# Kernel tuning notes

Hardware: AMD Instinct MI355X
Metric: run time of the kernel (lower is better)

Reference implementation:

```python
import jax, jax.numpy as jnp
import numpy as np

N_NODES = 50000
N_EDGES = 800000
F_NODE = 128
F_EDGE = 32
H = 64


def _gat_layer(x, row, col, e_emb, W, le_W, att_src, att_dst, att_edge, bias):
    """PyG GATConv (heads=1, concat=True) with edge_dim, incl. self loops.
    x: [N, Fin]; row/col: [E] int (src, dst); e_emb: [E, H].
    """
    N = x.shape[0]
    loop = jnp.arange(N, dtype=row.dtype)
    row_a = jnp.concatenate([row, loop])
    col_a = jnp.concatenate([col, loop])
    # self-loop edge attr = mean of edge embeddings (PyG fill_value='mean')
    e_mean = jnp.mean(e_emb, axis=0)
    e_all = jnp.concatenate([e_emb, jnp.broadcast_to(e_mean, (N, e_emb.shape[1]))], axis=0)

    h = x @ W.T                      # [N, H]
    a_src = h @ att_src              # [N]
    a_dst = h @ att_dst              # [N]
    a_edge = (e_all @ le_W.T) @ att_edge  # [E+N]

    alpha = jax.nn.leaky_relu(a_src[row_a] + a_dst[col_a] + a_edge, negative_slope=0.2)
    # segment softmax over destination node neighborhoods
    m = jax.ops.segment_max(alpha, col_a, num_segments=N)
    ex = jnp.exp(alpha - m[col_a])
    denom = jax.ops.segment_sum(ex, col_a, num_segments=N)
    w = ex / denom[col_a]            # [E+N]
    out = jax.ops.segment_sum(h[row_a] * w[:, None], col_a, num_segments=N)
    return out + bias


def setup_inputs() -> dict:
    key = jax.random.key(0)
    ks = jax.random.split(key, 20)
    s = 0.1
    inp = {
        "x": jax.random.normal(ks[0], (N_NODES, F_NODE), dtype=jnp.float32),
        "edge_attr": jax.random.normal(ks[1], (N_EDGES, F_EDGE), dtype=jnp.float32),
        "edge_index": jax.random.randint(ks[2], (2, N_EDGES), 0, N_NODES, dtype=jnp.int32),
        # edge encoder (Linear with bias)
        "enc_W": jax.random.normal(ks[3], (H, F_EDGE), dtype=jnp.float32) * s,
        "enc_b": jnp.zeros((H,), dtype=jnp.float32),
        # conv1 params
        "W1": jax.random.normal(ks[4], (H, F_NODE), dtype=jnp.float32) * s,
        "le1_W": jax.random.normal(ks[5], (H, H), dtype=jnp.float32) * s,
        "as1": jax.random.normal(ks[6], (H,), dtype=jnp.float32) * s,
        "ad1": jax.random.normal(ks[7], (H,), dtype=jnp.float32) * s,
        "ae1": jax.random.normal(ks[8], (H,), dtype=jnp.float32) * s,
        "b1": jnp.zeros((H,), dtype=jnp.float32),
        # conv2 params
        "W2": jax.random.normal(ks[9], (H, H), dtype=jnp.float32) * s,
        "le2_W": jax.random.normal(ks[10], (H, H), dtype=jnp.float32) * s,
        "as2": jax.random.normal(ks[11], (H,), dtype=jnp.float32) * s,
        "ad2": jax.random.normal(ks[12], (H,), dtype=jnp.float32) * s,
        "ae2": jax.random.normal(ks[13], (H,), dtype=jnp.float32) * s,
        "b2": jnp.zeros((H,), dtype=jnp.float32),
        # edge scorer MLP: Linear(2H, H) -> ReLU -> Linear(H, 1)
        "s1_W": jax.random.normal(ks[14], (H, 2 * H), dtype=jnp.float32) * s,
        "s1_b": jnp.zeros((H,), dtype=jnp.float32),
        "s2_W": jax.random.normal(ks[15], (1, H), dtype=jnp.float32) * s,
        "s2_b": jnp.zeros((1,), dtype=jnp.float32),
    }
    return inp


def reference(x, edge_attr, edge_index, enc_W, enc_b,
              W1, le1_W, as1, ad1, ae1, b1,
              W2, le2_W, as2, ad2, ae2, b2,
              s1_W, s1_b, s2_W, s2_b):
    row, col = edge_index[0], edge_index[1]
    edge_emb = edge_attr @ enc_W.T + enc_b           # [E, H]
    h = jax.nn.relu(_gat_layer(x, row, col, edge_emb, W1, le1_W, as1, ad1, ae1, b1))
    # dropout p=0.5 is identity in eval mode
    h = _gat_layer(h, row, col, edge_emb, W2, le2_W, as2, ad2, ae2, b2)
    ef = jnp.concatenate([h[row], h[col]], axis=1)   # [E, 2H]
    z = jax.nn.relu(ef @ s1_W.T + s1_b) @ s2_W.T + s2_b  # [E, 1]
    return jax.nn.sigmoid(z).squeeze(-1)             # [E]
```

## Files before the change

### kernel.cpp

```cpp
#include <hip/hip_runtime.h>
#include <cstdint>
#include <cstddef>

#define NN 50000
#define NE 800000
#define FN 128
#define FE 32
#define HD 64
#define SCAN_NB ((NN + 255) / 256)

__device__ __forceinline__ float lrelu(float x) { return x > 0.f ? x : 0.2f * x; }

__global__ void k_small0(const float* __restrict__ le1W, const float* __restrict__ ae1,
                         const float* __restrict__ le2W, const float* __restrict__ ae2,
                         const float* __restrict__ encW, const float* __restrict__ encb,
                         const float* __restrict__ s1W,
                         float* __restrict__ small, float* __restrict__ Scomb) {
  __shared__ float sv1[64], sv2[64];
  int t = threadIdx.x;
  float v1 = 0.f, v2 = 0.f;
  for (int j = 0; j < 64; ++j) {
    v1 += le1W[j * 64 + t] * ae1[j];
    v2 += le2W[j * 64 + t] * ae2[j];
  }
  sv1[t] = v1; sv2[t] = v2;
  small[t] = v1; small[64 + t] = v2;
  float cb1 = encb[t] * v1, cb2 = encb[t] * v2;
  #pragma unroll
  for (int m = 32; m; m >>= 1) { cb1 += __shfl_xor(cb1, m); cb2 += __shfl_xor(cb2, m); }
  __syncthreads();
  if (t < 32) {
    float p1 = 0.f, p2 = 0.f;
    for (int i = 0; i < 64; ++i) {
      p1 += encW[i * 32 + t] * sv1[i];
      p2 += encW[i * 32 + t] * sv2[i];
    }
    small[128 + t] = p1; small[160 + t] = p2;
  }
  if (t == 0) { small[192] = cb1; small[193] = cb2; }
  for (int j = 0; j < 64; ++j) {
    Scomb[j * 64 + t] = s1W[j * 128 + t];
    Scomb[(64 + j) * 64 + t] = s1W[j * 128 + 64 + t];
  }
}

__global__ __launch_bounds__(256) void k_scanA(const int* __restrict__ counts,
                                               int* __restrict__ loc, int* __restrict__ blocksums) {
  int tid = threadIdx.x;
  int i = blockIdx.x * 256 + tid;
  int v = (i < NN) ? counts[i] : 0;
  int lane = tid & 63, wid = tid >> 6;
  int x = v;
  #pragma unroll
  for (int d = 1; d < 64; d <<= 1) {
    int y = __shfl_up(x, d);
    if (lane >= d) x += y;
  }
  __shared__ int ws[4], wpref[4];
  if (lane == 63) ws[wid] = x;
  __syncthreads();
  if (tid == 0) {
    int run = 0;
    #pragma unroll
    for (int w = 0; w < 4; ++w) { wpref[w] = run; run += ws[w]; }
    blocksums[blockIdx.x] = run;
  }
  __syncthreads();
  if (i < NN) loc[i] = x - v + wpref[wid];
}

__global__ __launch_bounds__(256) void k_scanB(int* __restrict__ blocksums, int* __restrict__ offa,
                                               float* __restrict__ small) {
  int tid = threadIdx.x;
  int v = (tid < SCAN_NB) ? blocksums[tid] : 0;
  int lane = tid & 63, wid = tid >> 6;
  int x = v;
  #pragma unroll
  for (int d = 1; d < 64; d <<= 1) {
    int y = __shfl_up(x, d);
    if (lane >= d) x += y;
  }
  __shared__ int ws[4], wpref[4];
  if (lane == 63) ws[wid] = x;
  __syncthreads();
  if (tid == 0) {
    int run = 0;
    #pragma unroll
    for (int w = 0; w < 4; ++w) { wpref[w] = run; run += ws[w]; }
    offa[NN] = run;
    small[194] = small[228] * (1.0f / NE);
    small[195] = small[229] * (1.0f / NE);
  }
  __syncthreads();
  if (tid < SCAN_NB) blocksums[tid] = x - v + wpref[wid];
}

__global__ __launch_bounds__(256) void k_scanC(int* __restrict__ offa, const int* __restrict__ blocksums) {
  int i = blockIdx.x * 256 + threadIdx.x;
  if (i < NN) offa[i] = offa[i] + blocksums[blockIdx.x];
}

__global__ __launch_bounds__(256) void k_edgepre(const float* __restrict__ attr,
                                                 const int* __restrict__ col,
                                                 const float* __restrict__ small,
                                                 float* __restrict__ a_e1, float* __restrict__ a_e2,
                                                 int* __restrict__ rank,
                                                 int* __restrict__ counts,
                                                 float* __restrict__ sums) {
  __shared__ float sattr[256 * 33];
  __shared__ float redbuf[8];
  int tid = threadIdx.x;
  float sp1[32], sp2[32];
  #pragma unroll
  for (int j = 0; j < 8; ++j) {
    float4 v1 = ((const float4*)(small + 128))[j];
    float4 v2 = ((const float4*)(small + 160))[j];
    sp1[j*4+0] = v1.x; sp1[j*4+1] = v1.y; sp1[j*4+2] = v1.z; sp1[j*4+3] = v1.w;
    sp2[j*4+0] = v2.x; sp2[j*4+1] = v2.y; sp2[j*4+2] = v2.z; sp2[j*4+3] = v2.w;
  }
  float c1 = small[192], c2 = small[193];
  const float4* ain = (const float4*)(attr + (size_t)blockIdx.x * 256 * FE);
  #pragma unroll
  for (int it = 0; it < 8; ++it) {
    int idx = it * 256 + tid;
    float4 v = ain[idx];
    int r = idx >> 3, ch = idx & 7;
    float* dst = &sattr[r * 33 + ch * 4];
    dst[0] = v.x; dst[1] = v.y; dst[2] = v.z; dst[3] = v.w;
  }
  __syncthreads();
  const float* myrow = &sattr[tid * 33];
  float d1 = c1, d2 = c2;
  #pragma unroll
  for (int j = 0; j < 32; ++j) {
    float a = myrow[j];
    d1 += a * sp1[j];
    d2 += a * sp2[j];
  }
  int e = blockIdx.x * 256 + tid;
  a_e1[e] = d1;
  a_e2[e] = d2;
  int c = col[e];
  rank[e] = atomicAdd(&counts[c], 1);
  float s1 = d1, s2 = d2;
  #pragma unroll
  for (int m = 32; m; m >>= 1) { s1 += __shfl_xor(s1, m); s2 += __shfl_xor(s2, m); }
  int wid = tid >> 6;
  if ((tid & 63) == 0) { redbuf[wid] = s1; redbuf[4 + wid] = s2; }
  __syncthreads();
  if (tid == 0) atomicAdd(&sums[0], redbuf[0] + redbuf[1] + redbuf[2] + redbuf[3]);
  if (tid == 1) atomicAdd(&sums[1], redbuf[4] + redbuf[5] + redbuf[6] + redbuf[7]);
}

__global__ __launch_bounds__(256) void k_scatter(const int* __restrict__ row, const int* __restrict__ col,
                                                 const float* __restrict__ a_e1, const float* __restrict__ a_e2,
                                                 const int* __restrict__ rank, const int* __restrict__ offa,
                                                 int4* __restrict__ pk) {
  int e = blockIdx.x * 256 + threadIdx.x;
  int c = col[e];
  int p = offa[c] + rank[e];
  int4 q;
  q.x = row[e];
  q.y = __float_as_int(a_e1[e]);
  q.z = __float_as_int(a_e2[e]);
  q.w = 0;
  pk[p] = q;
}

template <int K, int ASD>
__global__ __launch_bounds__(256) void k_gemm(const float* __restrict__ A, const float* __restrict__ B,
                                              float* __restrict__ C, int M, int ldc,
                                              const float* __restrict__ as, const float* __restrict__ ad,
                                              float* __restrict__ asrc, float* __restrict__ adst) {
  __shared__ float At[64][68];
  __shared__ float Bt[64][68];
  int tid = threadIdx.x;
  int m0 = blockIdx.x * 64;
  const float* Bp = B + (size_t)blockIdx.y * 64 * K;
  float acc[4][4] = {};
  for (int kc = 0; kc < K; kc += 64) {
    #pragma unroll
    for (int it = 0; it < 4; ++it) {
      int idx = it * 256 + tid;
      int m = idx & 63, kv = idx >> 6;
      float4 bv = ((const float4*)(Bp + (size_t)m * K + kc))[kv];
      Bt[kv*4+0][m] = bv.x; Bt[kv*4+1][m] = bv.y; Bt[kv*4+2][m] = bv.z; Bt[kv*4+3][m] = bv.w;
      int gm = m0 + m;
      float4 av = make_float4(0.f, 0.f, 0.f, 0.f);
      if (gm < M) av = ((const float4*)(A + (size_t)gm * K + kc))[kv];
      At[kv*4+0][m] = av.x; At[kv*4+1][m] = av.y; At[kv*4+2][m] = av.z; At[kv*4+3][m] = av.w;
    }
    __syncthreads();
    int tn = tid & 15, tm = tid >> 4;
    #pragma unroll 8
    for (int k = 0; k < 64; ++k) {
      float4 a4 = *(const float4*)&At[k][tm * 4];
      float4 b4 = *(const float4*)&Bt[k][tn * 4];
      acc[0][0] += a4.x*b4.x; acc[0][1] += a4.x*b4.y; acc[0][2] += a4.x*b4.z; acc[0][3] += a4.x*b4.w;
      acc[1][0] += a4.y*b4.x; acc[1][1] += a4.y*b4.y; acc[1][2] += a4.y*b4.z; acc[1][3] += a4.y*b4.w;
      acc[2][0] += a4.z*b4.x; acc[2][1] += a4.z*b4.y; acc[2][2] += a4.z*b4.z; acc[2][3] += a4.z*b4.w;
      acc[3][0] += a4.w*b4.x; acc[3][1] += a4.w*b4.y; acc[3][2] += a4.w*b4.z; acc[3][3] += a4.w*b4.w;
    }
    __syncthreads();
  }
  int tn = tid & 15, tm = tid >> 4;
  #pragma unroll
  for (int i = 0; i < 4; ++i) {
    int gm = m0 + tm * 4 + i;
    if (gm < M) {
      float4 o = make_float4(acc[i][0], acc[i][1], acc[i][2], acc[i][3]);
      *(float4*)(C + (size_t)gm * ldc + blockIdx.y * 64 + tn * 4) = o;
    }
  }
  if constexpr (ASD) {
    float4 asv = ((const float4*)as)[tn];
    float4 adv = ((const float4*)ad)[tn];
    #pragma unroll
    for (int i = 0; i < 4; ++i) {
      float s = acc[i][0]*asv.x + acc[i][1]*asv.y + acc[i][2]*asv.z + acc[i][3]*asv.w;
      float d = acc[i][0]*adv.x + acc[i][1]*adv.y + acc[i][2]*adv.z + acc[i][3]*adv.w;
      #pragma unroll
      for (int m = 8; m; m >>= 1) { s += __shfl_xor(s, m, 16); d += __shfl_xor(d, m, 16); }
      int gm = m0 + tm * 4 + i;
      if (tn == 0 && gm < M) { asrc[gm] = s; adst[gm] = d; }
    }
  }
}

__global__ __launch_bounds__(256) void k_agg(const float* __restrict__ h, const int* __restrict__ offa,
                                             const int4* __restrict__ pk, int comp,
                                             const float* __restrict__ asrc, const float* __restrict__ adst,
                                             const float* __restrict__ small, int selfIdx,
                                             const float* __restrict__ bias, float* __restrict__ outp,
                                             int do_relu) {
  int gt = blockIdx.x * 256 + threadIdx.x;
  int n = gt >> 6, lane = gt & 63;
  if (n >= NN) return;
  int beg = offa[n], end = offa[n + 1];
  float a_self = small[selfIdx];
  float adn = adst[n];
  float alpha_self = lrelu(asrc[n] + adn + a_self);
  float mx = alpha_self;
  for (int base = beg; base < end; base += 64) {
    int p = base + lane;
    if (p < end) {
      int4 q = pk[p];
      float ae = __int_as_float(comp ? q.z : q.y);
      float al = lrelu(asrc[q.x] + adn + ae);
      mx = fmaxf(mx, al);
    }
  }
  #pragma unroll
  for (int m = 32; m; m >>= 1) mx = fmaxf(mx, __shfl_xor(mx, m));
  float ex_self = __expf(alpha_self - mx);
  float denom = ex_self;
  float acc = ex_self * h[(size_t)n * 64 + lane];
  for (int base = beg; base < end; base += 64) {
    int p = base + lane;
    int cnt = min(64, end - base);
    float ex = 0.f; int s = 0;
    if (p < end) {
      int4 q = pk[p];
      s = q.x;
      float ae = __int_as_float(comp ? q.z : q.y);
      ex = __expf(lrelu(asrc[s] + adn + ae) - mx);
    }
    float exs = ex;
    #pragma unroll
    for (int m = 32; m; m >>= 1) exs += __shfl_xor(exs, m);
    denom += exs;
    for (int q = 0; q < cnt; ++q) {
      float exq = __shfl(ex, q);
      int sq = __shfl(s, q);
      acc += exq * h[(size_t)sq * 64 + lane];
    }
  }
  float r = acc / denom + bias[lane];
  if (do_relu) r = fmaxf(r, 0.f);
  outp[(size_t)n * 64 + lane] = r;
}

__global__ __launch_bounds__(256) void k_final(const int* __restrict__ row, const int* __restrict__ col,
                                               const float* __restrict__ uv, const float* __restrict__ s1b,
                                               const float* __restrict__ s2w, const float* __restrict__ s2b,
                                               float* __restrict__ outp) {
  int gt = blockIdx.x * 256 + threadIdx.x;
  int e = gt >> 4, i = gt & 15;
  if (e >= NE) return;
  int r = row[e], c = col[e];
  float4 a = ((const float4*)(uv + (size_t)r * 128))[i];
  float4 b = ((const float4*)(uv + (size_t)c * 128 + 64))[i];
  float4 bb = ((const float4*)s1b)[i];
  float4 ww = ((const float4*)s2w)[i];
  float z = fmaxf(a.x + b.x + bb.x, 0.f) * ww.x
          + fmaxf(a.y + b.y + bb.y, 0.f) * ww.y
          + fmaxf(a.z + b.z + bb.z, 0.f) * ww.z
          + fmaxf(a.w + b.w + bb.w, 0.f) * ww.w;
  #pragma unroll
  for (int m = 1; m < 16; m <<= 1) z += __shfl_xor(z, m, 16);
  if (i == 0) outp[e] = 1.f / (1.f + __expf(-(z + s2b[0])));
}

extern "C" void kernel_launch(void* const* d_in, const int* in_sizes, int n_in,
                              void* d_out, int out_size, void* d_ws, size_t ws_size,
                              hipStream_t stream) {
  const float* x    = (const float*)d_in[0];
  const float* attr = (const float*)d_in[1];
  const int*   eidx = (const int*)d_in[2];
  const float* encW = (const float*)d_in[3];
  const float* encb = (const float*)d_in[4];
  const float* W1   = (const float*)d_in[5];
  const float* le1W = (const float*)d_in[6];
  const float* as1  = (const float*)d_in[7];
  const float* ad1  = (const float*)d_in[8];
  const float* ae1w = (const float*)d_in[9];
  const float* b1   = (const float*)d_in[10];
  const float* W2   = (const float*)d_in[11];
  const float* le2W = (const float*)d_in[12];
  const float* as2  = (const float*)d_in[13];
  const float* ad2  = (const float*)d_in[14];
  const float* ae2w = (const float*)d_in[15];
  const float* b2   = (const float*)d_in[16];
  const float* s1W  = (const float*)d_in[17];
  const float* s1b  = (const float*)d_in[18];
  const float* s2w  = (const float*)d_in[19];
  const float* s2b  = (const float*)d_in[20];
  float* outp = (float*)d_out;

  const int* row = eidx;
  const int* col = eidx + NE;

  char* p = (char*)d_ws;
  auto alloc = [&](size_t bytes) { char* r = p; p += (bytes + 255) & ~(size_t)255; return r; };
  float* small = (float*)alloc(1024);
  float* Scomb = (float*)alloc(8192 * 4);
  int*   counts= (int*)alloc((size_t)NN * 4);
  int*   offa  = (int*)alloc((size_t)(NN + 1) * 4);
  int*   bsums = (int*)alloc((size_t)SCAN_NB * 4);
  float* a_e1  = (float*)alloc((size_t)NE * 4);
  float* a_e2  = (float*)alloc((size_t)NE * 4);
  int*   rank  = (int*)alloc((size_t)NE * 4);
  int4*  pk    = (int4*)alloc((size_t)NE * 16);
  float* h1    = (float*)alloc((size_t)NN * 64 * 4);
  float* out1  = (float*)alloc((size_t)NN * 64 * 4);
  float* h2    = (float*)alloc((size_t)NN * 64 * 4);
  float* out2  = (float*)alloc((size_t)NN * 64 * 4);
  float* asrc1 = (float*)alloc((size_t)NN * 4);
  float* adst1 = (float*)alloc((size_t)NN * 4);
  float* asrc2 = (float*)alloc((size_t)NN * 4);
  float* adst2 = (float*)alloc((size_t)NN * 4);
  float* uv = h1;

  hipMemsetAsync(small, 0, 1024, stream);
  hipMemsetAsync(counts, 0, (size_t)NN * 4, stream);

  k_small0<<<1, 64, 0, stream>>>(le1W, ae1w, le2W, ae2w, encW, encb, s1W, small, Scomb);
  k_edgepre<<<NE / 256, 256, 0, stream>>>(attr, col, small, a_e1, a_e2, rank, counts, small + 228);
  k_scanA<<<SCAN_NB, 256, 0, stream>>>(counts, offa, bsums);
  k_scanB<<<1, 256, 0, stream>>>(bsums, offa, small);
  k_scanC<<<SCAN_NB, 256, 0, stream>>>(offa, bsums);
  k_scatter<<<NE / 256, 256, 0, stream>>>(row, col, a_e1, a_e2, rank, offa, pk);

  k_gemm<128, 1><<<dim3((NN + 63) / 64, 1), 256, 0, stream>>>(x, W1, h1, NN, 64, as1, ad1, asrc1, adst1);
  k_agg<<<(NN * 64) / 256, 256, 0, stream>>>(h1, offa, pk, 0, asrc1, adst1,
                                             small, 194, b1, out1, 1);
  k_gemm<64, 1><<<dim3((NN + 63) / 64, 1), 256, 0, stream>>>(out1, W2, h2, NN, 64, as2, ad2, asrc2, adst2);
  k_agg<<<(NN * 64) / 256, 256, 0, stream>>>(h2, offa, pk, 1, asrc2, adst2,
                                             small, 195, b2, out2, 0);
  k_gemm<64, 0><<<dim3((NN + 63) / 64, 2), 256, 0, stream>>>(out2, Scomb, uv, NN, 128, nullptr, nullptr, nullptr, nullptr);
  k_final<<<(NE * 16) / 256, 256, 0, stream>>>(row, col, uv, s1b, s2w, s2b, outp);
}
```

Measured before the change: 368.8 us.

## Replace global atomic rank counting with per-block LDS histograms and prefix reduction

Edge ranking within destination buckets moves out of the edge-preprocessing kernel, where it used global atomics on counts, into a dedicated histogram kernel. Each of 256 blocks builds 16-bit packed shared-memory histograms in two node-range phases, and a node-reduction kernel prefix-sums the per-block histograms to produce counts and per-block offsets. The scatter kernel then combines the block prefix with a local 16-bit rank. This removes contended global atomics and the counts memset, but adds two kernel launches, a 25.6 MB histogram buffer that reuses h1, and a serial 256-step column walk in the reduction kernel.

```diff
diff --git a/kernel.cpp b/kernel.cpp
--- a/kernel.cpp
+++ b/kernel.cpp
@@ -8,6 +8,9 @@
 #define FE 32
 #define HD 64
 #define SCAN_NB ((NN + 255) / 256)
+#define NB_H 256
+#define EPB_H (NE / NB_H)
+#define NWORD 25000
 
 __device__ __forceinline__ float lrelu(float x) { return x > 0.f ? x : 0.2f * x; }
 
@@ -44,6 +47,49 @@
   }
 }
 
+__global__ __launch_bounds__(256) void k_hist(const int* __restrict__ col,
+                                              uint32_t* __restrict__ histg,
+                                              unsigned short* __restrict__ rankw) {
+  __shared__ uint32_t h32[NWORD / 2];
+  int tid = threadIdx.x;
+  int b = blockIdx.x;
+  int e0 = b * EPB_H;
+  #pragma unroll
+  for (int ph = 0; ph < 2; ++ph) {
+    for (int i = tid; i < NWORD / 2; i += 256) h32[i] = 0;
+    __syncthreads();
+    int lo = ph * 25000;
+    for (int i = tid; i < EPB_H; i += 256) {
+      int c = col[e0 + i];
+      unsigned local = (unsigned)(c - lo);
+      if (local < 25000u) {
+        uint32_t sh = (local & 1u) * 16u;
+        uint32_t old = atomicAdd(&h32[local >> 1], 1u << sh);
+        rankw[e0 + i] = (unsigned short)((old >> sh) & 0xffffu);
+      }
+    }
+    __syncthreads();
+    uint32_t* dst = histg + (size_t)b * NWORD + ph * (NWORD / 2);
+    for (int i = tid; i < NWORD / 2; i += 256) dst[i] = h32[i];
+    __syncthreads();
+  }
+}
+
+__global__ __launch_bounds__(256) void k_nodered(uint32_t* __restrict__ histg,
+                                                 int* __restrict__ counts) {
+  int w = blockIdx.x * 256 + threadIdx.x;
+  if (w >= NWORD) return;
+  uint32_t run = 0;
+  for (int b = 0; b < NB_H; ++b) {
+    uint32_t* p = histg + (size_t)b * NWORD + w;
+    uint32_t v = *p;
+    *p = run;
+    run += v;
+  }
+  counts[2 * w] = (int)(run & 0xffffu);
+  counts[2 * w + 1] = (int)(run >> 16);
+}
+
 __global__ __launch_bounds__(256) void k_scanA(const int* __restrict__ counts,
                                                int* __restrict__ loc, int* __restrict__ blocksums) {
   int tid = threadIdx.x;
@@ -101,11 +147,8 @@
 }
 
 __global__ __launch_bounds__(256) void k_edgepre(const float* __restrict__ attr,
-                                                 const int* __restrict__ col,
                                                  const float* __restrict__ small,
                                                  float* __restrict__ a_e1, float* __restrict__ a_e2,
-                                                 int* __restrict__ rank,
-                                                 int* __restrict__ counts,
                                                  float* __restrict__ sums) {
   __shared__ float sattr[256 * 33];
   __shared__ float redbuf[8];
@@ -140,8 +183,6 @@
   int e = blockIdx.x * 256 + tid;
   a_e1[e] = d1;
   a_e2[e] = d2;
-  int c = col[e];
-  rank[e] = atomicAdd(&counts[c], 1);
   float s1 = d1, s2 = d2;
   #pragma unroll
   for (int m = 32; m; m >>= 1) { s1 += __shfl_xor(s1, m); s2 += __shfl_xor(s2, m); }
@@ -154,11 +195,15 @@
 
 __global__ __launch_bounds__(256) void k_scatter(const int* __restrict__ row, const int* __restrict__ col,
                                                  const float* __restrict__ a_e1, const float* __restrict__ a_e2,
-                                                 const int* __restrict__ rank, const int* __restrict__ offa,
+                                                 const unsigned short* __restrict__ rankw,
+                                                 const uint32_t* __restrict__ histg,
+                                                 const int* __restrict__ offa,
                                                  int4* __restrict__ pk) {
   int e = blockIdx.x * 256 + threadIdx.x;
   int c = col[e];
-  int p = offa[c] + rank[e];
+  int b = e / EPB_H;
+  int pre = (int)((const unsigned short*)histg)[(size_t)b * (2 * NWORD) + c];
+  int p = offa[c] + pre + (int)rankw[e];
   int4 q;
   q.x = row[e];
   q.y = __float_as_int(a_e1[e]);
@@ -339,7 +384,7 @@
   int*   bsums = (int*)alloc((size_t)SCAN_NB * 4);
   float* a_e1  = (float*)alloc((size_t)NE * 4);
   float* a_e2  = (float*)alloc((size_t)NE * 4);
-  int*   rank  = (int*)alloc((size_t)NE * 4);
+  unsigned short* rankw = (unsigned short*)alloc((size_t)NE * 2);
   int4*  pk    = (int4*)alloc((size_t)NE * 16);
   float* h1    = (float*)alloc((size_t)NN * 64 * 4);
   float* out1  = (float*)alloc((size_t)NN * 64 * 4);
@@ -350,16 +395,18 @@
   float* asrc2 = (float*)alloc((size_t)NN * 4);
   float* adst2 = (float*)alloc((size_t)NN * 4);
   float* uv = h1;
+  uint32_t* histg = (uint32_t*)h1;
 
   hipMemsetAsync(small, 0, 1024, stream);
-  hipMemsetAsync(counts, 0, (size_t)NN * 4, stream);
 
   k_small0<<<1, 64, 0, stream>>>(le1W, ae1w, le2W, ae2w, encW, encb, s1W, small, Scomb);
-  k_edgepre<<<NE / 256, 256, 0, stream>>>(attr, col, small, a_e1, a_e2, rank, counts, small + 228);
+  k_edgepre<<<NE / 256, 256, 0, stream>>>(attr, small, a_e1, a_e2, small + 228);
+  k_hist<<<NB_H, 256, 0, stream>>>(col, histg, rankw);
+  k_nodered<<<(NWORD + 255) / 256, 256, 0, stream>>>(histg, counts);
   k_scanA<<<SCAN_NB, 256, 0, stream>>>(counts, offa, bsums);
   k_scanB<<<1, 256, 0, stream>>>(bsums, offa, small);
   k_scanC<<<SCAN_NB, 256, 0, stream>>>(offa, bsums);
-  k_scatter<<<NE / 256, 256, 0, stream>>>(row, col, a_e1, a_e2, rank, offa, pk);
+  k_scatter<<<NE / 256, 256, 0, stream>>>(row, col, a_e1, a_e2, rankw, histg, offa, pk);
 
   k_gemm<128, 1><<<dim3((NN + 63) / 64, 1), 256, 0, stream>>>(x, W1, h1, NN, 64, as1, ad1, asrc1, adst1);
   k_agg<<<(NN * 64) / 256, 256, 0, stream>>>(h1, offa, pk, 0, asrc1, adst1,
```

Result: slower. 392.3 us (+6.4%).

## Replace per-node softmax max pass with global upper-bound max from atomics

Applied to the files above, without the earlier changes.

Drops the per-node first pass over incoming edges that computed the exact segment max. Instead, an upper bound on the max is built from global maxima of a_src and a_edge, gathered with ordered-int atomicMax in the GEMM and edge-prep kernels, and passed through leaky ReLU. Softmax is invariant to the shift, so this removes one full gather pass over the edges per layer. It risks underflow in exp when a node's logits sit far below the global bound, and it adds a block sync plus an atomic per GEMM block. The self-loop edge term is not included in the bound.

```diff
diff --git a/kernel.cpp b/kernel.cpp
--- a/kernel.cpp
+++ b/kernel.cpp
@@ -10,6 +10,14 @@
 #define SCAN_NB ((NN + 255) / 256)
 
 __device__ __forceinline__ float lrelu(float x) { return x > 0.f ? x : 0.2f * x; }
+
+__device__ __forceinline__ unsigned omap(float f) {
+  unsigned u = __float_as_uint(f);
+  return (u & 0x80000000u) ? ~u : (u | 0x80000000u);
+}
+__device__ __forceinline__ float odec(unsigned u) {
+  return __uint_as_float((u & 0x80000000u) ? (u ^ 0x80000000u) : ~u);
+}
 
 __global__ void k_small0(const float* __restrict__ le1W, const float* __restrict__ ae1,
                          const float* __restrict__ le2W, const float* __restrict__ ae2,
@@ -106,9 +114,10 @@
                                                  float* __restrict__ a_e1, float* __restrict__ a_e2,
                                                  int* __restrict__ rank,
                                                  int* __restrict__ counts,
-                                                 float* __restrict__ sums) {
+                                                 float* __restrict__ sums,
+                                                 unsigned* __restrict__ maxi) {
   __shared__ float sattr[256 * 33];
-  __shared__ float redbuf[8];
+  __shared__ float redbuf[16];
   int tid = threadIdx.x;
   float sp1[32], sp2[32];
   #pragma unroll
@@ -142,14 +151,19 @@
   a_e2[e] = d2;
   int c = col[e];
   rank[e] = atomicAdd(&counts[c], 1);
-  float s1 = d1, s2 = d2;
-  #pragma unroll
-  for (int m = 32; m; m >>= 1) { s1 += __shfl_xor(s1, m); s2 += __shfl_xor(s2, m); }
+  float s1 = d1, s2 = d2, m1 = d1, m2 = d2;
+  #pragma unroll
+  for (int m = 32; m; m >>= 1) {
+    s1 += __shfl_xor(s1, m); s2 += __shfl_xor(s2, m);
+    m1 = fmaxf(m1, __shfl_xor(m1, m)); m2 = fmaxf(m2, __shfl_xor(m2, m));
+  }
   int wid = tid >> 6;
-  if ((tid & 63) == 0) { redbuf[wid] = s1; redbuf[4 + wid] = s2; }
+  if ((tid & 63) == 0) { redbuf[wid] = s1; redbuf[4 + wid] = s2; redbuf[8 + wid] = m1; redbuf[12 + wid] = m2; }
   __syncthreads();
   if (tid == 0) atomicAdd(&sums[0], redbuf[0] + redbuf[1] + redbuf[2] + redbuf[3]);
   if (tid == 1) atomicAdd(&sums[1], redbuf[4] + redbuf[5] + redbuf[6] + redbuf[7]);
+  if (tid == 2) atomicMax(&maxi[2], omap(fmaxf(fmaxf(redbuf[8], redbuf[9]), fmaxf(redbuf[10], redbuf[11]))));
+  if (tid == 3) atomicMax(&maxi[3], omap(fmaxf(fmaxf(redbuf[12], redbuf[13]), fmaxf(redbuf[14], redbuf[15]))));
 }
 
 __global__ __launch_bounds__(256) void k_scatter(const int* __restrict__ row, const int* __restrict__ col,
@@ -171,7 +185,8 @@
 __global__ __launch_bounds__(256) void k_gemm(const float* __restrict__ A, const float* __restrict__ B,
                                               float* __restrict__ C, int M, int ldc,
                                               const float* __restrict__ as, const float* __restrict__ ad,
-                                              float* __restrict__ asrc, float* __restrict__ adst) {
+                                              float* __restrict__ asrc, float* __restrict__ adst,
+                                              unsigned* __restrict__ maxslot) {
   __shared__ float At[64][68];
   __shared__ float Bt[64][68];
   int tid = threadIdx.x;
@@ -213,8 +228,10 @@
     }
   }
   if constexpr (ASD) {
+    __shared__ float wmax[4];
     float4 asv = ((const float4*)as)[tn];
     float4 adv = ((const float4*)ad)[tn];
+    float smax = -1e30f;
     #pragma unroll
     for (int i = 0; i < 4; ++i) {
       float s = acc[i][0]*asv.x + acc[i][1]*asv.y + acc[i][2]*asv.z + acc[i][3]*asv.w;
@@ -222,8 +239,14 @@
       #pragma unroll
       for (int m = 8; m; m >>= 1) { s += __shfl_xor(s, m, 16); d += __shfl_xor(d, m, 16); }
       int gm = m0 + tm * 4 + i;
-      if (tn == 0 && gm < M) { asrc[gm] = s; adst[gm] = d; }
-    }
+      if (tn == 0 && gm < M) { asrc[gm] = s; adst[gm] = d; smax = fmaxf(smax, s); }
+    }
+    #pragma unroll
+    for (int m = 32; m; m >>= 1) smax = fmaxf(smax, __shfl_xor(smax, m));
+    if ((tid & 63) == 0) wmax[tid >> 6] = smax;
+    __syncthreads();
+    if (tid == 0)
+      atomicMax(maxslot, omap(fmaxf(fmaxf(wmax[0], wmax[1]), fmaxf(wmax[2], wmax[3]))));
   }
 }
 
@@ -231,6 +254,7 @@
                                              const int4* __restrict__ pk, int comp,
                                              const float* __restrict__ asrc, const float* __restrict__ adst,
                                              const float* __restrict__ small, int selfIdx,
+                                             const unsigned* __restrict__ maxi,
                                              const float* __restrict__ bias, float* __restrict__ outp,
                                              int do_relu) {
   int gt = blockIdx.x * 256 + threadIdx.x;
@@ -239,19 +263,8 @@
   int beg = offa[n], end = offa[n + 1];
   float a_self = small[selfIdx];
   float adn = adst[n];
+  float mx = lrelu(odec(maxi[comp]) + adn + odec(maxi[2 + comp]));
   float alpha_self = lrelu(asrc[n] + adn + a_self);
-  float mx = alpha_self;
-  for (int base = beg; base < end; base += 64) {
-    int p = base + lane;
-    if (p < end) {
-      int4 q = pk[p];
-      float ae = __int_as_float(comp ? q.z : q.y);
-      float al = lrelu(asrc[q.x] + adn + ae);
-      mx = fmaxf(mx, al);
-    }
-  }
-  #pragma unroll
-  for (int m = 32; m; m >>= 1) mx = fmaxf(mx, __shfl_xor(mx, m));
   float ex_self = __expf(alpha_self - mx);
   float denom = ex_self;
   float acc = ex_self * h[(size_t)n * 64 + lane];
@@ -333,6 +346,7 @@
   char* p = (char*)d_ws;
   auto alloc = [&](size_t bytes) { char* r = p; p += (bytes + 255) & ~(size_t)255; return r; };
   float* small = (float*)alloc(1024);
+  unsigned* maxi = (unsigned*)alloc(256);
   float* Scomb = (float*)alloc(8192 * 4);
   int*   counts= (int*)alloc((size_t)NN * 4);
   int*   offa  = (int*)alloc((size_t)(NN + 1) * 4);
@@ -352,21 +366,22 @@
   float* uv = h1;
 
   hipMemsetAsync(small, 0, 1024, stream);
+  hipMemsetAsync(maxi, 0, 256, stream);
   hipMemsetAsync(counts, 0, (size_t)NN * 4, stream);
 
   k_small0<<<1, 64, 0, stream>>>(le1W, ae1w, le2W, ae2w, encW, encb, s1W, small, Scomb);
-  k_edgepre<<<NE / 256, 256, 0, stream>>>(attr, col, small, a_e1, a_e2, rank, counts, small + 228);
+  k_edgepre<<<NE / 256, 256, 0, stream>>>(attr, col, small, a_e1, a_e2, rank, counts, small + 228, maxi);
   k_scanA<<<SCAN_NB, 256, 0, stream>>>(counts, offa, bsums);
   k_scanB<<<1, 256, 0, stream>>>(bsums, offa, small);
   k_scanC<<<SCAN_NB, 256, 0, stream>>>(offa, bsums);
   k_scatter<<<NE / 256, 256, 0, stream>>>(row, col, a_e1, a_e2, rank, offa, pk);
 
-  k_gemm<128, 1><<<dim3((NN + 63) / 64, 1), 256, 0, stream>>>(x, W1, h1, NN, 64, as1, ad1, asrc1, adst1);
+  k_gemm<128, 1><<<dim3((NN + 63) / 64, 1), 256, 0, stream>>>(x, W1, h1, NN, 64, as1, ad1, asrc1, adst1, maxi + 0);
   k_agg<<<(NN * 64) / 256, 256, 0, stream>>>(h1, offa, pk, 0, asrc1, adst1,
-                                             small, 194, b1, out1, 1);
-  k_gemm<64, 1><<<dim3((NN + 63) / 64, 1), 256, 0, stream>>>(out1, W2, h2, NN, 64, as2, ad2, asrc2, adst2);
+                                             small, 194, maxi, b1, out1, 1);
+  k_gemm<64, 1><<<dim3((NN + 63) / 64, 1), 256, 0, stream>>>(out1, W2, h2, NN, 64, as2, ad2, asrc2, adst2, maxi + 1);
   k_agg<<<(NN * 64) / 256, 256, 0, stream>>>(h2, offa, pk, 1, asrc2, adst2,
-                                             small, 195, b2, out2, 0);
-  k_gemm<64, 0><<<dim3((NN + 63) / 64, 2), 256, 0, stream>>>(out2, Scomb, uv, NN, 128, nullptr, nullptr, nullptr, nullptr);
+                                             small, 195, maxi, b2, out2, 0);
+  k_gemm<64, 0><<<dim3((NN + 63) / 64, 2), 256, 0, stream>>>(out2, Scomb, uv, NN, 128, nullptr, nullptr, nullptr, nullptr, nullptr);
   k_final<<<(NE * 16) / 256, 256, 0, stream>>>(row, col, uv, s1b, s2w, s2b, outp);
 }
```

Result: no change. 374.5 us (+1.6%).
